# Kernel tuning notes

Hardware: AMD Instinct MI355X
Metric: run time of the kernel (lower is better)

Reference implementation:

```python
import jax, jax.numpy as jnp
import numpy as np

B, TQ, TK, D, H = 8, 1024, 1024, 1024, 16
HD = D // H
EPS = 1e-5


def layernorm(x, g, b):
    mu = jnp.mean(x, axis=-1, keepdims=True)
    var = jnp.mean(jnp.square(x - mu), axis=-1, keepdims=True)
    return (x - mu) * jax.lax.rsqrt(var + EPS) * g + b


def setup_inputs() -> dict:
    key = jax.random.key(0)
    ks = jax.random.split(key, 16)
    s = 1.0 / np.sqrt(D)
    return {
        "base": jax.random.normal(ks[0], (B, TQ, D), jnp.float32),
        "fusion": jax.random.normal(ks[1], (B, TK, D), jnp.float32),
        "Wq": jax.random.normal(ks[2], (D, D), jnp.float32) * s,
        "Wk": jax.random.normal(ks[3], (D, D), jnp.float32) * s,
        "Wv": jax.random.normal(ks[4], (D, D), jnp.float32) * s,
        "Wo": jax.random.normal(ks[5], (D, D), jnp.float32) * s,
        "g1": jnp.ones((D,), jnp.float32),
        "b1": jnp.zeros((D,), jnp.float32),
        "g2": jnp.ones((D,), jnp.float32),
        "b2": jnp.zeros((D,), jnp.float32),
        "fc1_w": jax.random.normal(ks[6], (D, D), jnp.float32) * s,
        "fc1_b": jnp.zeros((D,), jnp.float32),
        "fc2_w": jax.random.normal(ks[7], (D, D), jnp.float32) * s,
        "fc2_b": jnp.zeros((D,), jnp.float32),
        "rw": jax.random.normal(ks[8], (D, D), jnp.float32) * s,
        "rb": jnp.zeros((D,), jnp.float32),
        "alpha": jnp.asarray(0.1, jnp.float32),
    }


def reference(base, fusion, Wq, Wk, Wv, Wo, g1, b1, g2, b2,
              fc1_w, fc1_b, fc2_w, fc2_b, rw, rb, alpha):
    def split_heads(x):  # [B,T,D] -> [B,H,T,hd]
        return x.reshape(B, -1, H, HD).transpose(0, 2, 1, 3)

    Q = split_heads(base @ Wq.T)
    K = split_heads(fusion @ Wk.T)
    V = split_heads(fusion @ Wv.T)

    scores = jnp.einsum("bhqd,bhkd->bhqk", Q, K) / jnp.sqrt(jnp.float32(HD))
    attn = jax.nn.softmax(scores, axis=-1)
    # threshold mask (the torch scatter_ with arange indices is an identity copy)
    masked = attn * (attn >= alpha).astype(attn.dtype)
    # second softmax over masked weights (zeros contribute exp(0)=1, as in the original)
    attn2 = jax.nn.softmax(masked, axis=-1)
    out = jnp.einsum("bhqk,bhkd->bhqd", attn2, V)
    out = out.transpose(0, 2, 1, 3).reshape(B, TQ, D)
    out = out @ Wo.T
    x = layernorm(base + out, g1, b1)  # dropout is eval-mode identity
    ff = jax.nn.silu(jax.nn.silu(x @ fc1_w.T + fc1_b) @ fc2_w.T + fc2_b)
    y = layernorm(x + ff, g2, b2)
    final = y @ rw.T + rb
    return final, masked
```

## Files before the change

### kernel.cpp

```cpp
#include <hip/hip_runtime.h>


typedef unsigned short u16;
typedef __attribute__((ext_vector_type(8))) short  bf16x8;
typedef __attribute__((ext_vector_type(4))) short  s16x4;
typedef __attribute__((ext_vector_type(4))) float  f32x4;

#define GLL16(gp, lp) __builtin_amdgcn_global_load_lds(                     \
    (__attribute__((address_space(1))) const void*)(gp),                    \
    (__attribute__((address_space(3))) void*)(lp), 16, 0, 0)

__device__ __forceinline__ u16 f2bf(float x) {
  union { float f; unsigned u; } v; v.f = x;
  return (u16)((v.u + 0x7FFF + ((v.u >> 16) & 1)) >> 16);
}
__device__ __forceinline__ float bf2f(u16 h) {
  union { unsigned u; float f; } v; v.u = ((unsigned)h) << 16;
  return v.f;
}
__device__ __forceinline__ f32x4 zero4() { f32x4 z = {0.f, 0.f, 0.f, 0.f}; return z; }

__global__ __launch_bounds__(256) void pack_act(const float* __restrict__ a,
                                                const float* __restrict__ b,
                                                u16* __restrict__ outa,
                                                u16* __restrict__ outb) {
  size_t i = (size_t)blockIdx.x * 256 + threadIdx.x;
  const f32x4* in = (const f32x4*)(blockIdx.y ? b : a);
  s16x4* out = (s16x4*)(blockIdx.y ? outb : outa);
  f32x4 v = in[i];
  s16x4 o;
  o[0] = (short)f2bf(v[0]); o[1] = (short)f2bf(v[1]);
  o[2] = (short)f2bf(v[2]); o[3] = (short)f2bf(v[3]);
  out[i] = o;
}

__global__ __launch_bounds__(256) void pack_w(
    const float* __restrict__ w0, const float* __restrict__ w1,
    const float* __restrict__ w2, const float* __restrict__ w3,
    const float* __restrict__ w4, const float* __restrict__ w5,
    const float* __restrict__ w6, u16* __restrict__ out) {
  size_t i = (size_t)blockIdx.x * 256 + threadIdx.x;
  const float* in;
  switch (blockIdx.y) {
    case 0: in = w0; break;  case 1: in = w1; break;
    case 2: in = w2; break;  case 3: in = w3; break;
    case 4: in = w4; break;  case 5: in = w5; break;
    default: in = w6; break;
  }
  f32x4 v = ((const f32x4*)in)[i];
  s16x4 o;
  o[0] = (short)f2bf(v[0]); o[1] = (short)f2bf(v[1]);
  o[2] = (short)f2bf(v[2]); o[3] = (short)f2bf(v[3]);
  ((s16x4*)(out + (size_t)blockIdx.y * 1048576))[i] = o;
}

#define EPI_QKV       0
#define EPI_BF16      1
#define EPI_SILU_BF16 4
#define EPI_BIAS_F32  6

template <int EPI>
__global__ __launch_bounds__(256) void gemm_bt(
    const u16* __restrict__ A, int lda,
    const u16* __restrict__ W, int ldw,
    int M, int N, int K,
    float* __restrict__ outF, u16* __restrict__ outU,
    const float* __restrict__ bias,
    const u16* __restrict__ A2) {
  __shared__ u16 As[2][128 * 32];
  __shared__ u16 Bs[2][128 * 32];
  int tid = threadIdx.x;
  int l = tid & 63, w = tid >> 6;
  int wr = w >> 1, wc = w & 1, lr = l & 15, lq = l >> 4;

  int fid = blockIdx.y * 8 + blockIdx.x;
  int swz = (fid & 7) * 64 + (fid >> 3);
  int m0 = (swz >> 3) * 128, n0 = (swz & 7) * 128;

  const u16* Ap = A;
  const u16* Wp = W;
  u16* outUp = outU;
  if constexpr (EPI == EPI_QKV) {
    int z = blockIdx.z;
    if (z) Ap = A2;
    Wp = W + (size_t)z * 1048576;
    outUp = outU + (size_t)z * 8388608;
  }

  f32x4 acc[4][4];
#pragma unroll
  for (int i = 0; i < 4; i++)
#pragma unroll
    for (int j = 0; j < 4; j++) acc[i][j] = zero4();

  auto stage = [&](const u16* src, int ld, int r0, int k0, u16* lds) {
#pragma unroll
    for (int j = 0; j < 2; ++j) {
      int seg = j * 256 + tid;
      int row = seg >> 2, sp = seg & 3;
      const u16* g = src + (size_t)(r0 + row) * ld + k0 +
                     ((sp ^ ((row >> 1) & 3)) << 3);
      GLL16(g, lds + seg * 8);
    }
  };

  int nk = K >> 5;
  stage(Ap, lda, m0, 0, As[0]);
  stage(Wp, ldw, n0, 0, Bs[0]);
  for (int kt = 0; kt < nk; ++kt) {
    __syncthreads();
    if (kt + 1 < nk) {
      stage(Ap, lda, m0, (kt + 1) << 5, As[(kt + 1) & 1]);
      stage(Wp, ldw, n0, (kt + 1) << 5, Bs[(kt + 1) & 1]);
    }
    const u16* Ab = As[kt & 1];
    const u16* Bb = Bs[kt & 1];
    bf16x8 af[4], bw[4];
    int slot = (lq ^ ((lr >> 1) & 3)) << 3;
#pragma unroll
    for (int mi = 0; mi < 4; mi++)
      af[mi] = *(const bf16x8*)&Ab[(wr * 64 + mi * 16 + lr) * 32 + slot];
#pragma unroll
    for (int ni = 0; ni < 4; ni++)
      bw[ni] = *(const bf16x8*)&Bb[(wc * 64 + ni * 16 + lr) * 32 + slot];
#pragma unroll
    for (int mi = 0; mi < 4; mi++)
#pragma unroll
      for (int ni = 0; ni < 4; ni++)
        acc[mi][ni] = __builtin_amdgcn_mfma_f32_16x16x32_bf16(af[mi], bw[ni],
                                                              acc[mi][ni], 0, 0, 0);
  }

#pragma unroll
  for (int mi = 0; mi < 4; mi++) {
#pragma unroll
    for (int ni = 0; ni < 4; ni++) {
      int col = n0 + wc * 64 + ni * 16 + lr;
#pragma unroll
      for (int r = 0; r < 4; r++) {
        int row = m0 + wr * 64 + mi * 16 + lq * 4 + r;
        float v = acc[mi][ni][r];
        if constexpr (EPI == EPI_QKV) {
          int b = row >> 10, t = row & 1023, h = col >> 6, d = col & 63;
          int z = blockIdx.z;
          if (z == 0) {
            outUp[((size_t)(b * 16 + h) * 1024 + t) * 64 + d] = f2bf(v);
          } else if (z == 1) {
            size_t base = ((size_t)(b * 16 + h) * 1024 + t) * 64;
            outUp[base + (((d >> 3) ^ (t & 7)) << 3) + (d & 7)] = f2bf(v);
          } else {
            size_t o = ((size_t)(b * 16 + h) * 64 + d) * 1024 + (t & ~63) +
                       ((((t >> 3) & 7) ^ (d & 7)) << 3) + (t & 7);
            outUp[o] = f2bf(v);
          }
        } else if constexpr (EPI == EPI_BF16) {
          outUp[(size_t)row * N + col] = f2bf(v);
        } else if constexpr (EPI == EPI_SILU_BF16) {
          float z = v + bias[col];
          outUp[(size_t)row * N + col] = f2bf(z / (1.f + __expf(-z)));
        } else {
          outF[(size_t)row * N + col] = v + bias[col];
        }
      }
    }
  }
}

template <int EPI>
__global__ __launch_bounds__(512) void gemm_bt8(
    const u16* __restrict__ A, int lda,
    const u16* __restrict__ W, int ldw,
    int M, int N, int K,
    float* __restrict__ outF, u16* __restrict__ outU,
    const float* __restrict__ bias) {
  __shared__ u16 As[2][128 * 32];
  __shared__ u16 Bs[2][128 * 32];
  int tid = threadIdx.x;
  int l = tid & 63, w = tid >> 6;
  int wr = w >> 2, wc = w & 3, lr = l & 15, lq = l >> 4;

  int fid = blockIdx.y * 8 + blockIdx.x;
  int swz = (fid & 7) * 64 + (fid >> 3);
  int m0 = (swz >> 3) * 128, n0 = (swz & 7) * 128;

  f32x4 acc[4][2];
#pragma unroll
  for (int i = 0; i < 4; i++)
#pragma unroll
    for (int j = 0; j < 2; j++) acc[i][j] = zero4();

  auto stage = [&](const u16* src, int ld, int r0, int k0, u16* lds) {
    int seg = tid;
    int row = seg >> 2, sp = seg & 3;
    const u16* g = src + (size_t)(r0 + row) * ld + k0 +
                   ((sp ^ ((row >> 1) & 3)) << 3);
    GLL16(g, lds + seg * 8);
  };

  int nk = K >> 5;
  stage(A, lda, m0, 0, As[0]);
  stage(W, ldw, n0, 0, Bs[0]);
  for (int kt = 0; kt < nk; ++kt) {
    __syncthreads();
    if (kt + 1 < nk) {
      stage(A, lda, m0, (kt + 1) << 5, As[(kt + 1) & 1]);
      stage(W, ldw, n0, (kt + 1) << 5, Bs[(kt + 1) & 1]);
    }
    const u16* Ab = As[kt & 1];
    const u16* Bb = Bs[kt & 1];
    bf16x8 af[4], bw[2];
    int slot = (lq ^ ((lr >> 1) & 3)) << 3;
#pragma unroll
    for (int mi = 0; mi < 4; mi++)
      af[mi] = *(const bf16x8*)&Ab[(wr * 64 + mi * 16 + lr) * 32 + slot];
#pragma unroll
    for (int ni = 0; ni < 2; ni++)
      bw[ni] = *(const bf16x8*)&Bb[(wc * 32 + ni * 16 + lr) * 32 + slot];
#pragma unroll
    for (int mi = 0; mi < 4; mi++)
#pragma unroll
      for (int ni = 0; ni < 2; ni++)
        acc[mi][ni] = __builtin_amdgcn_mfma_f32_16x16x32_bf16(af[mi], bw[ni],
                                                              acc[mi][ni], 0, 0, 0);
  }

#pragma unroll
  for (int mi = 0; mi < 4; mi++) {
#pragma unroll
    for (int ni = 0; ni < 2; ni++) {
      int col = n0 + wc * 32 + ni * 16 + lr;
#pragma unroll
      for (int r = 0; r < 4; r++) {
        int row = m0 + wr * 64 + mi * 16 + lq * 4 + r;
        float v = acc[mi][ni][r];
        if constexpr (EPI == EPI_BF16) {
          outU[(size_t)row * N + col] = f2bf(v);
        } else if constexpr (EPI == EPI_SILU_BF16) {
          float z = v + bias[col];
          outU[(size_t)row * N + col] = f2bf(z / (1.f + __expf(-z)));
        } else {
          outF[(size_t)row * N + col] = v + bias[col];
        }
      }
    }
  }
}

__global__ __launch_bounds__(256) void attn_kernel(
    const u16* __restrict__ Q2, const u16* __restrict__ K2,
    const u16* __restrict__ Vt, const float* __restrict__ alphap,
    float* __restrict__ masked_out, u16* __restrict__ attn_out) {
  __shared__ __align__(16) u16 Ks[2][4096];
  __shared__ __align__(16) u16 Vs[2][4096];
  __shared__ __align__(16) u16 Ps[4][2][16 * 72];

  int tid = threadIdx.x;
  int l = tid & 63, w = tid >> 6, lr = l & 15, lq = l >> 4;

  int bid = blockIdx.x;
  int qi  = bid >> 7;
  int bh  = (bid & 7) * 16 + ((bid >> 3) & 15);
  int h = bh & 15, b = bh >> 4;
  int q0 = qi * 128;

  const u16* Qb = Q2 + (size_t)bh * 1024 * 64;
  const u16* Kb = K2 + (size_t)bh * 1024 * 64;
  const u16* Vb = Vt + (size_t)bh * 64 * 1024;
  float alpha = alphap[0];
  int qw = q0 + w * 32;

  auto stageK = [&](int kc, u16* dst) {
#pragma unroll
    for (int j = 0; j < 2; ++j) {
      int seg = j * 256 + tid;
      GLL16(Kb + (size_t)kc * 4096 + seg * 8, dst + seg * 8);
    }
  };
  auto stageV = [&](int kc, u16* dst) {
#pragma unroll
    for (int j = 0; j < 2; ++j) {
      int seg = j * 256 + tid;
      GLL16(Vb + (size_t)(seg >> 3) * 1024 + kc * 64 + (seg & 7) * 8, dst + seg * 8);
    }
  };

  bf16x8 qf[2][2];
#pragma unroll
  for (int s = 0; s < 2; s++)
#pragma unroll
    for (int kt = 0; kt < 2; kt++)
      qf[s][kt] = *(const bf16x8*)(Qb + (size_t)(qw + s * 16 + lr) * 64 + kt * 32 + lq * 8);

  float s1[2][4] = {{0.f, 0.f, 0.f, 0.f}, {0.f, 0.f, 0.f, 0.f}};

  stageK(0, Ks[0]);
  for (int kc = 0; kc < 16; ++kc) {
    __syncthreads();
    if (kc + 1 < 16) stageK(kc + 1, Ks[(kc + 1) & 1]);
    const u16* Kc = Ks[kc & 1];
    f32x4 acc[2][4];
#pragma unroll
    for (int s = 0; s < 2; s++)
#pragma unroll
      for (int ni = 0; ni < 4; ni++) acc[s][ni] = zero4();
    __builtin_amdgcn_s_setprio(1);
#pragma unroll
    for (int ni = 0; ni < 4; ++ni) {
      int t = ni * 16 + lr;
      bf16x8 k0 = *(const bf16x8*)&Kc[t * 64 + (((0 + lq) ^ (lr & 7)) << 3)];
      bf16x8 k1 = *(const bf16x8*)&Kc[t * 64 + (((4 + lq) ^ (lr & 7)) << 3)];
#pragma unroll
      for (int s = 0; s < 2; s++) {
        acc[s][ni] = __builtin_amdgcn_mfma_f32_16x16x32_bf16(qf[s][0], k0, acc[s][ni], 0, 0, 0);
        acc[s][ni] = __builtin_amdgcn_mfma_f32_16x16x32_bf16(qf[s][1], k1, acc[s][ni], 0, 0, 0);
      }
    }
    __builtin_amdgcn_s_setprio(0);
#pragma unroll
    for (int s = 0; s < 2; s++)
#pragma unroll
      for (int ni = 0; ni < 4; ni++)
#pragma unroll
        for (int r = 0; r < 4; r++)
          s1[s][r] += __expf(acc[s][ni][r] * 0.125f);
  }
#pragma unroll
  for (int s = 0; s < 2; s++)
#pragma unroll
    for (int r = 0; r < 4; r++) {
      float v = s1[s][r];
      v += __shfl_xor(v, 1); v += __shfl_xor(v, 2);
      v += __shfl_xor(v, 4); v += __shfl_xor(v, 8);
      s1[s][r] = 1.0f / v;
    }

  float s2[2][4] = {{0.f, 0.f, 0.f, 0.f}, {0.f, 0.f, 0.f, 0.f}};
  f32x4 oacc[2][4];
#pragma unroll
  for (int s = 0; s < 2; s++)
#pragma unroll
    for (int dg = 0; dg < 4; dg++) oacc[s][dg] = zero4();

  stageK(0, Ks[0]);
  stageV(0, Vs[0]);
  for (int kc = 0; kc < 16; ++kc) {
    if (kc == 0) {
      asm volatile("s_waitcnt vmcnt(0) lgkmcnt(0)" ::: "memory");
    } else {
      asm volatile("s_waitcnt vmcnt(32) lgkmcnt(0)" ::: "memory");
    }
    __builtin_amdgcn_s_barrier();
    __builtin_amdgcn_sched_barrier(0);
    if (kc + 1 < 16) {
      stageK(kc + 1, Ks[(kc + 1) & 1]);
      stageV(kc + 1, Vs[(kc + 1) & 1]);
    }
    const u16* Kc = Ks[kc & 1];
    const u16* Vc = Vs[kc & 1];

    f32x4 acc[2][4];
#pragma unroll
    for (int s = 0; s < 2; s++)
#pragma unroll
      for (int ni = 0; ni < 4; ni++) acc[s][ni] = zero4();
    __builtin_amdgcn_s_setprio(1);
#pragma unroll
    for (int ni = 0; ni < 4; ++ni) {
      int t = ni * 16 + lr;
      bf16x8 k0 = *(const bf16x8*)&Kc[t * 64 + (((0 + lq) ^ (lr & 7)) << 3)];
      bf16x8 k1 = *(const bf16x8*)&Kc[t * 64 + (((4 + lq) ^ (lr & 7)) << 3)];
#pragma unroll
      for (int s = 0; s < 2; s++) {
        acc[s][ni] = __builtin_amdgcn_mfma_f32_16x16x32_bf16(qf[s][0], k0, acc[s][ni], 0, 0, 0);
        acc[s][ni] = __builtin_amdgcn_mfma_f32_16x16x32_bf16(qf[s][1], k1, acc[s][ni], 0, 0, 0);
      }
    }
    __builtin_amdgcn_s_setprio(0);

#pragma unroll
    for (int s = 0; s < 2; s++) {
#pragma unroll
      for (int ni = 0; ni < 4; ni++) {
#pragma unroll
        for (int r = 0; r < 4; r++) {
          float e = __expf(acc[s][ni][r] * 0.125f);
          float a = e * s1[s][r];
          a = (a >= alpha) ? a : 0.0f;
          size_t row = (size_t)bh * 1024 + qw + s * 16 + lq * 4 + r;
          masked_out[row * 1024 + kc * 64 + ni * 16 + lr] = a;
          float p = __expf(a);
          s2[s][r] += p;
          Ps[w][s][(lq * 4 + r) * 72 + ni * 16 + lr] = f2bf(p);
        }
      }
    }
    asm volatile("s_waitcnt lgkmcnt(0)" ::: "memory");

    bf16x8 pf[2][2];
#pragma unroll
    for (int s = 0; s < 2; s++)
#pragma unroll
      for (int kt = 0; kt < 2; kt++)
        pf[s][kt] = *(const bf16x8*)&Ps[w][s][lr * 72 + kt * 32 + lq * 8];
    __builtin_amdgcn_s_setprio(1);
#pragma unroll
    for (int dg = 0; dg < 4; dg++) {
      int d = dg * 16 + lr;
      bf16x8 v0 = *(const bf16x8*)&Vc[d * 64 + (((0 + lq) ^ (lr & 7)) << 3)];
      bf16x8 v1 = *(const bf16x8*)&Vc[d * 64 + (((4 + lq) ^ (lr & 7)) << 3)];
#pragma unroll
      for (int s = 0; s < 2; s++) {
        oacc[s][dg] = __builtin_amdgcn_mfma_f32_16x16x32_bf16(pf[s][0], v0, oacc[s][dg], 0, 0, 0);
        oacc[s][dg] = __builtin_amdgcn_mfma_f32_16x16x32_bf16(pf[s][1], v1, oacc[s][dg], 0, 0, 0);
      }
    }
    __builtin_amdgcn_s_setprio(0);
  }

#pragma unroll
  for (int s = 0; s < 2; s++)
#pragma unroll
    for (int r = 0; r < 4; r++) {
      float v = s2[s][r];
      v += __shfl_xor(v, 1); v += __shfl_xor(v, 2);
      v += __shfl_xor(v, 4); v += __shfl_xor(v, 8);
      s2[s][r] = 1.0f / v;
    }
#pragma unroll
  for (int s = 0; s < 2; s++)
#pragma unroll
    for (int dg = 0; dg < 4; dg++)
#pragma unroll
      for (int r = 0; r < 4; r++) {
        int q = qw + s * 16 + lq * 4 + r;
        attn_out[(size_t)(b * 1024 + q) * 1024 + h * 64 + dg * 16 + lr] =
            f2bf(oacc[s][dg][r] * s2[s][r]);
      }
}

__global__ __launch_bounds__(256) void ln_kernel(
    const float* __restrict__ A, const u16* __restrict__ Bv,
    const float* __restrict__ g, const float* __restrict__ beta,
    float* __restrict__ outF, u16* __restrict__ outB) {
  __shared__ float red[4];
  int row = blockIdx.x, t = threadIdx.x;
  const float* pa = A + (size_t)row * 1024;
  const u16* pb = Bv + (size_t)row * 1024;
  float v[4];
  float s = 0.f;
#pragma unroll
  for (int i = 0; i < 4; i++) {
    int c = t + 256 * i;
    v[i] = pa[c] + bf2f(pb[c]);
    s += v[i];
  }
#pragma unroll
  for (int off = 1; off < 64; off <<= 1) s += __shfl_xor(s, off);
  if ((t & 63) == 0) red[t >> 6] = s;
  __syncthreads();
  s = red[0] + red[1] + red[2] + red[3];
  float mu = s * 0.0009765625f;
  float q = 0.f;
#pragma unroll
  for (int i = 0; i < 4; i++) { float d = v[i] - mu; q += d * d; }
  __syncthreads();
#pragma unroll
  for (int off = 1; off < 64; off <<= 1) q += __shfl_xor(q, off);
  if ((t & 63) == 0) red[t >> 6] = q;
  __syncthreads();
  q = red[0] + red[1] + red[2] + red[3];
  float rs = rsqrtf(q * 0.0009765625f + 1e-5f);
#pragma unroll
  for (int i = 0; i < 4; i++) {
    int c = t + 256 * i;
    float y = (v[i] - mu) * rs * g[c] + beta[c];
    if (outF) outF[(size_t)row * 1024 + c] = y;
    if (outB) outB[(size_t)row * 1024 + c] = f2bf(y);
  }
}

#define WS_BASEB   0
#define WS_FUSB    16777216
#define WS_W       33554432
#define WS_QKV     48234496
#define WS_ATTNO   98566144
#define WS_X       115343360
#define WS_OB      WS_FUSB
#define WS_XB      WS_BASEB
#define WS_H1      WS_ATTNO
#define WS_FFB     WS_QKV
#define WS_YB      (WS_QKV + 16777216)

extern "C" void kernel_launch(void* const* d_in, const int* in_sizes, int n_in,
                              void* d_out, int out_size, void* d_ws, size_t ws_size,
                              hipStream_t stream) {
  const float* base   = (const float*)d_in[0];
  const float* fusion = (const float*)d_in[1];
  const float* Wq     = (const float*)d_in[2];
  const float* Wk     = (const float*)d_in[3];
  const float* Wv     = (const float*)d_in[4];
  const float* Wo     = (const float*)d_in[5];
  const float* g1     = (const float*)d_in[6];
  const float* b1     = (const float*)d_in[7];
  const float* g2     = (const float*)d_in[8];
  const float* b2     = (const float*)d_in[9];
  const float* fc1w   = (const float*)d_in[10];
  const float* fc1b   = (const float*)d_in[11];
  const float* fc2w   = (const float*)d_in[12];
  const float* fc2b   = (const float*)d_in[13];
  const float* rw     = (const float*)d_in[14];
  const float* rb     = (const float*)d_in[15];
  const float* alphap = (const float*)d_in[16];

  char* ws = (char*)d_ws;
  u16* baseb  = (u16*)(ws + WS_BASEB);
  u16* fusb   = (u16*)(ws + WS_FUSB);
  u16* wall   = (u16*)(ws + WS_W);
  u16* Q2     = (u16*)(ws + WS_QKV);
  u16* attno  = (u16*)(ws + WS_ATTNO);
  u16* obufb  = (u16*)(ws + WS_OB);
  float* x    = (float*)(ws + WS_X);
  u16* xb     = (u16*)(ws + WS_XB);
  u16* h1     = (u16*)(ws + WS_H1);
  u16* ffb    = (u16*)(ws + WS_FFB);
  u16* yb     = (u16*)(ws + WS_YB);

  float* final_out  = (float*)d_out;
  float* masked_out = final_out + 8388608;

  pack_act<<<dim3(8192, 2), 256, 0, stream>>>(base, fusion, baseb, fusb);
  pack_w<<<dim3(1024, 7), 256, 0, stream>>>(Wq, Wk, Wv, Wo, fc1w, fc2w, rw, wall);

  dim3 gg(8, 64);

  gemm_bt<EPI_QKV><<<dim3(8, 64, 3), 256, 0, stream>>>(
      baseb, 1024, wall, 1024, 8192, 1024, 1024, nullptr, Q2, nullptr, fusb);

  attn_kernel<<<dim3(1024), 256, 0, stream>>>(
      Q2, Q2 + 8388608, Q2 + 16777216, alphap, masked_out, attno);

  gemm_bt8<EPI_BF16><<<gg, 512, 0, stream>>>(attno, 1024, wall + 3 * 1048576, 1024,
                                             8192, 1024, 1024, nullptr, obufb, nullptr);
  ln_kernel<<<8192, 256, 0, stream>>>(base, obufb, g1, b1, x, xb);

  gemm_bt8<EPI_SILU_BF16><<<gg, 512, 0, stream>>>(xb, 1024, wall + 4 * 1048576, 1024,
                                                  8192, 1024, 1024, nullptr, h1, fc1b);
  gemm_bt8<EPI_SILU_BF16><<<gg, 512, 0, stream>>>(h1, 1024, wall + 5 * 1048576, 1024,
                                                  8192, 1024, 1024, nullptr, ffb, fc2b);
  ln_kernel<<<8192, 256, 0, stream>>>(x, ffb, g2, b2, nullptr, yb);

  gemm_bt8<EPI_BIAS_F32><<<gg, 512, 0, stream>>>(yb, 1024, wall + 6 * 1048576, 1024,
                                                 8192, 1024, 1024, final_out, nullptr, rb);
}
```

Measured before the change: 977.2 us.

## Double GEMM K-tile and split attention across eight waves per block

The bt8 GEMM now stages 64-wide K tiles with an 8-way XOR swizzle, halving the number of barrier/pipeline iterations per output tile. The attention kernel uses 512 threads with each wave owning 16 query rows instead of 32, adjusting staging, wait counts and the P scratch buffer. This aims to raise occupancy and latency hiding in attention and reduce sync overhead in the GEMMs, at the cost of more LDS per GEMM block and lower per-wave reuse of K/V fragments in attention.

```diff
diff --git a/kernel.cpp b/kernel.cpp
--- a/kernel.cpp
+++ b/kernel.cpp
@@ -173,8 +173,8 @@
     int M, int N, int K,
     float* __restrict__ outF, u16* __restrict__ outU,
     const float* __restrict__ bias) {
-  __shared__ u16 As[2][128 * 32];
-  __shared__ u16 Bs[2][128 * 32];
+  __shared__ u16 As[2][128 * 64];
+  __shared__ u16 Bs[2][128 * 64];
   int tid = threadIdx.x;
   int l = tid & 63, w = tid >> 6;
   int wr = w >> 2, wc = w & 3, lr = l & 15, lq = l >> 4;
@@ -190,38 +190,46 @@
     for (int j = 0; j < 2; j++) acc[i][j] = zero4();
 
   auto stage = [&](const u16* src, int ld, int r0, int k0, u16* lds) {
-    int seg = tid;
-    int row = seg >> 2, sp = seg & 3;
-    const u16* g = src + (size_t)(r0 + row) * ld + k0 +
-                   ((sp ^ ((row >> 1) & 3)) << 3);
-    GLL16(g, lds + seg * 8);
+#pragma unroll
+    for (int j = 0; j < 2; ++j) {
+      int seg = j * 512 + tid;
+      int row = seg >> 3, sp = seg & 7;
+      const u16* g = src + (size_t)(r0 + row) * ld + k0 +
+                     ((sp ^ (row & 7)) << 3);
+      GLL16(g, lds + seg * 8);
+    }
   };
 
-  int nk = K >> 5;
+  int nk = K >> 6;
   stage(A, lda, m0, 0, As[0]);
   stage(W, ldw, n0, 0, Bs[0]);
   for (int kt = 0; kt < nk; ++kt) {
     __syncthreads();
     if (kt + 1 < nk) {
-      stage(A, lda, m0, (kt + 1) << 5, As[(kt + 1) & 1]);
-      stage(W, ldw, n0, (kt + 1) << 5, Bs[(kt + 1) & 1]);
+      stage(A, lda, m0, (kt + 1) << 6, As[(kt + 1) & 1]);
+      stage(W, ldw, n0, (kt + 1) << 6, Bs[(kt + 1) & 1]);
     }
     const u16* Ab = As[kt & 1];
     const u16* Bb = Bs[kt & 1];
-    bf16x8 af[4], bw[2];
-    int slot = (lq ^ ((lr >> 1) & 3)) << 3;
-#pragma unroll
-    for (int mi = 0; mi < 4; mi++)
-      af[mi] = *(const bf16x8*)&Ab[(wr * 64 + mi * 16 + lr) * 32 + slot];
-#pragma unroll
-    for (int ni = 0; ni < 2; ni++)
-      bw[ni] = *(const bf16x8*)&Bb[(wc * 32 + ni * 16 + lr) * 32 + slot];
-#pragma unroll
-    for (int mi = 0; mi < 4; mi++)
+    bf16x8 af[4][2], bw[2][2];
+#pragma unroll
+    for (int kk = 0; kk < 2; kk++) {
+      int slot = ((kk * 4 + lq) ^ (lr & 7)) << 3;
+#pragma unroll
+      for (int mi = 0; mi < 4; mi++)
+        af[mi][kk] = *(const bf16x8*)&Ab[(wr * 64 + mi * 16 + lr) * 64 + slot];
 #pragma unroll
       for (int ni = 0; ni < 2; ni++)
-        acc[mi][ni] = __builtin_amdgcn_mfma_f32_16x16x32_bf16(af[mi], bw[ni],
-                                                              acc[mi][ni], 0, 0, 0);
+        bw[ni][kk] = *(const bf16x8*)&Bb[(wc * 32 + ni * 16 + lr) * 64 + slot];
+    }
+#pragma unroll
+    for (int kk = 0; kk < 2; kk++)
+#pragma unroll
+      for (int mi = 0; mi < 4; mi++)
+#pragma unroll
+        for (int ni = 0; ni < 2; ni++)
+          acc[mi][ni] = __builtin_amdgcn_mfma_f32_16x16x32_bf16(
+              af[mi][kk], bw[ni][kk], acc[mi][ni], 0, 0, 0);
   }
 
 #pragma unroll
@@ -246,13 +254,13 @@
   }
 }
 
-__global__ __launch_bounds__(256) void attn_kernel(
+__global__ __launch_bounds__(512) void attn_kernel(
     const u16* __restrict__ Q2, const u16* __restrict__ K2,
     const u16* __restrict__ Vt, const float* __restrict__ alphap,
     float* __restrict__ masked_out, u16* __restrict__ attn_out) {
   __shared__ __align__(16) u16 Ks[2][4096];
   __shared__ __align__(16) u16 Vs[2][4096];
-  __shared__ __align__(16) u16 Ps[4][2][16 * 72];
+  __shared__ __align__(16) u16 Ps[8][16 * 72];
 
   int tid = threadIdx.x;
   int l = tid & 63, w = tid >> 6, lr = l & 15, lq = l >> 4;
@@ -267,79 +275,60 @@
   const u16* Kb = K2 + (size_t)bh * 1024 * 64;
   const u16* Vb = Vt + (size_t)bh * 64 * 1024;
   float alpha = alphap[0];
-  int qw = q0 + w * 32;
+  int qw = q0 + w * 16;
 
   auto stageK = [&](int kc, u16* dst) {
-#pragma unroll
-    for (int j = 0; j < 2; ++j) {
-      int seg = j * 256 + tid;
-      GLL16(Kb + (size_t)kc * 4096 + seg * 8, dst + seg * 8);
-    }
+    int seg = tid;
+    GLL16(Kb + (size_t)kc * 4096 + seg * 8, dst + seg * 8);
   };
   auto stageV = [&](int kc, u16* dst) {
-#pragma unroll
-    for (int j = 0; j < 2; ++j) {
-      int seg = j * 256 + tid;
-      GLL16(Vb + (size_t)(seg >> 3) * 1024 + kc * 64 + (seg & 7) * 8, dst + seg * 8);
-    }
+    int seg = tid;
+    GLL16(Vb + (size_t)(seg >> 3) * 1024 + kc * 64 + (seg & 7) * 8, dst + seg * 8);
   };
 
-  bf16x8 qf[2][2];
-#pragma unroll
-  for (int s = 0; s < 2; s++)
-#pragma unroll
-    for (int kt = 0; kt < 2; kt++)
-      qf[s][kt] = *(const bf16x8*)(Qb + (size_t)(qw + s * 16 + lr) * 64 + kt * 32 + lq * 8);
-
-  float s1[2][4] = {{0.f, 0.f, 0.f, 0.f}, {0.f, 0.f, 0.f, 0.f}};
+  bf16x8 qf[2];
+#pragma unroll
+  for (int kt = 0; kt < 2; kt++)
+    qf[kt] = *(const bf16x8*)(Qb + (size_t)(qw + lr) * 64 + kt * 32 + lq * 8);
+
+  float s1[4] = {0.f, 0.f, 0.f, 0.f};
 
   stageK(0, Ks[0]);
   for (int kc = 0; kc < 16; ++kc) {
     __syncthreads();
     if (kc + 1 < 16) stageK(kc + 1, Ks[(kc + 1) & 1]);
     const u16* Kc = Ks[kc & 1];
-    f32x4 acc[2][4];
-#pragma unroll
-    for (int s = 0; s < 2; s++)
-#pragma unroll
-      for (int ni = 0; ni < 4; ni++) acc[s][ni] = zero4();
+    f32x4 acc[4];
+#pragma unroll
+    for (int ni = 0; ni < 4; ni++) acc[ni] = zero4();
     __builtin_amdgcn_s_setprio(1);
 #pragma unroll
     for (int ni = 0; ni < 4; ++ni) {
       int t = ni * 16 + lr;
       bf16x8 k0 = *(const bf16x8*)&Kc[t * 64 + (((0 + lq) ^ (lr & 7)) << 3)];
       bf16x8 k1 = *(const bf16x8*)&Kc[t * 64 + (((4 + lq) ^ (lr & 7)) << 3)];
-#pragma unroll
-      for (int s = 0; s < 2; s++) {
-        acc[s][ni] = __builtin_amdgcn_mfma_f32_16x16x32_bf16(qf[s][0], k0, acc[s][ni], 0, 0, 0);
-        acc[s][ni] = __builtin_amdgcn_mfma_f32_16x16x32_bf16(qf[s][1], k1, acc[s][ni], 0, 0, 0);
-      }
+      acc[ni] = __builtin_amdgcn_mfma_f32_16x16x32_bf16(qf[0], k0, acc[ni], 0, 0, 0);
+      acc[ni] = __builtin_amdgcn_mfma_f32_16x16x32_bf16(qf[1], k1, acc[ni], 0, 0, 0);
     }
     __builtin_amdgcn_s_setprio(0);
 #pragma unroll
-    for (int s = 0; s < 2; s++)
-#pragma unroll
-      for (int ni = 0; ni < 4; ni++)
-#pragma unroll
-        for (int r = 0; r < 4; r++)
-          s1[s][r] += __expf(acc[s][ni][r] * 0.125f);
-  }
-#pragma unroll
-  for (int s = 0; s < 2; s++)
-#pragma unroll
-    for (int r = 0; r < 4; r++) {
-      float v = s1[s][r];
-      v += __shfl_xor(v, 1); v += __shfl_xor(v, 2);
-      v += __shfl_xor(v, 4); v += __shfl_xor(v, 8);
-      s1[s][r] = 1.0f / v;
-    }
-
-  float s2[2][4] = {{0.f, 0.f, 0.f, 0.f}, {0.f, 0.f, 0.f, 0.f}};
-  f32x4 oacc[2][4];
-#pragma unroll
-  for (int s = 0; s < 2; s++)
-#pragma unroll
-    for (int dg = 0; dg < 4; dg++) oacc[s][dg] = zero4();
+    for (int ni = 0; ni < 4; ni++)
+#pragma unroll
+      for (int r = 0; r < 4; r++)
+        s1[r] += __expf(acc[ni][r] * 0.125f);
+  }
+#pragma unroll
+  for (int r = 0; r < 4; r++) {
+    float v = s1[r];
+    v += __shfl_xor(v, 1); v += __shfl_xor(v, 2);
+    v += __shfl_xor(v, 4); v += __shfl_xor(v, 8);
+    s1[r] = 1.0f / v;
+  }
+
+  float s2[4] = {0.f, 0.f, 0.f, 0.f};
+  f32x4 oacc[4];
+#pragma unroll
+  for (int dg = 0; dg < 4; dg++) oacc[dg] = zero4();
 
   stageK(0, Ks[0]);
   stageV(0, Vs[0]);
@@ -347,7 +336,7 @@
     if (kc == 0) {
       asm volatile("s_waitcnt vmcnt(0) lgkmcnt(0)" ::: "memory");
     } else {
-      asm volatile("s_waitcnt vmcnt(32) lgkmcnt(0)" ::: "memory");
+      asm volatile("s_waitcnt vmcnt(16) lgkmcnt(0)" ::: "memory");
     }
     __builtin_amdgcn_s_barrier();
     __builtin_amdgcn_sched_barrier(0);
@@ -358,84 +347,67 @@
     const u16* Kc = Ks[kc & 1];
     const u16* Vc = Vs[kc & 1];
 
-    f32x4 acc[2][4];
-#pragma unroll
-    for (int s = 0; s < 2; s++)
-#pragma unroll
-      for (int ni = 0; ni < 4; ni++) acc[s][ni] = zero4();
+    f32x4 acc[4];
+#pragma unroll
+    for (int ni = 0; ni < 4; ni++) acc[ni] = zero4();
     __builtin_amdgcn_s_setprio(1);
 #pragma unroll
     for (int ni = 0; ni < 4; ++ni) {
       int t = ni * 16 + lr;
       bf16x8 k0 = *(const bf16x8*)&Kc[t * 64 + (((0 + lq) ^ (lr & 7)) << 3)];
       bf16x8 k1 = *(const bf16x8*)&Kc[t * 64 + (((4 + lq) ^ (lr & 7)) << 3)];
-#pragma unroll
-      for (int s = 0; s < 2; s++) {
-        acc[s][ni] = __builtin_amdgcn_mfma_f32_16x16x32_bf16(qf[s][0], k0, acc[s][ni], 0, 0, 0);
-        acc[s][ni] = __builtin_amdgcn_mfma_f32_16x16x32_bf16(qf[s][1], k1, acc[s][ni], 0, 0, 0);
+      acc[ni] = __builtin_amdgcn_mfma_f32_16x16x32_bf16(qf[0], k0, acc[ni], 0, 0, 0);
+      acc[ni] = __builtin_amdgcn_mfma_f32_16x16x32_bf16(qf[1], k1, acc[ni], 0, 0, 0);
+    }
+    __builtin_amdgcn_s_setprio(0);
+
+#pragma unroll
+    for (int ni = 0; ni < 4; ni++) {
+#pragma unroll
+      for (int r = 0; r < 4; r++) {
+        float e = __expf(acc[ni][r] * 0.125f);
+        float a = e * s1[r];
+        a = (a >= alpha) ? a : 0.0f;
+        size_t row = (size_t)bh * 1024 + qw + lq * 4 + r;
+        masked_out[row * 1024 + kc * 64 + ni * 16 + lr] = a;
+        float p = __expf(a);
+        s2[r] += p;
+        Ps[w][(lq * 4 + r) * 72 + ni * 16 + lr] = f2bf(p);
       }
     }
-    __builtin_amdgcn_s_setprio(0);
-
-#pragma unroll
-    for (int s = 0; s < 2; s++) {
-#pragma unroll
-      for (int ni = 0; ni < 4; ni++) {
-#pragma unroll
-        for (int r = 0; r < 4; r++) {
-          float e = __expf(acc[s][ni][r] * 0.125f);
-          float a = e * s1[s][r];
-          a = (a >= alpha) ? a : 0.0f;
-          size_t row = (size_t)bh * 1024 + qw + s * 16 + lq * 4 + r;
-          masked_out[row * 1024 + kc * 64 + ni * 16 + lr] = a;
-          float p = __expf(a);
-          s2[s][r] += p;
-          Ps[w][s][(lq * 4 + r) * 72 + ni * 16 + lr] = f2bf(p);
-        }
-      }
-    }
     asm volatile("s_waitcnt lgkmcnt(0)" ::: "memory");
 
-    bf16x8 pf[2][2];
-#pragma unroll
-    for (int s = 0; s < 2; s++)
-#pragma unroll
-      for (int kt = 0; kt < 2; kt++)
-        pf[s][kt] = *(const bf16x8*)&Ps[w][s][lr * 72 + kt * 32 + lq * 8];
+    bf16x8 pf[2];
+#pragma unroll
+    for (int kt = 0; kt < 2; kt++)
+      pf[kt] = *(const bf16x8*)&Ps[w][lr * 72 + kt * 32 + lq * 8];
     __builtin_amdgcn_s_setprio(1);
 #pragma unroll
     for (int dg = 0; dg < 4; dg++) {
       int d = dg * 16 + lr;
       bf16x8 v0 = *(const bf16x8*)&Vc[d * 64 + (((0 + lq) ^ (lr & 7)) << 3)];
       bf16x8 v1 = *(const bf16x8*)&Vc[d * 64 + (((4 + lq) ^ (lr & 7)) << 3)];
-#pragma unroll
-      for (int s = 0; s < 2; s++) {
-        oacc[s][dg] = __builtin_amdgcn_mfma_f32_16x16x32_bf16(pf[s][0], v0, oacc[s][dg], 0, 0, 0);
-        oacc[s][dg] = __builtin_amdgcn_mfma_f32_16x16x32_bf16(pf[s][1], v1, oacc[s][dg], 0, 0, 0);
-      }
+      oacc[dg] = __builtin_amdgcn_mfma_f32_16x16x32_bf16(pf[0], v0, oacc[dg], 0, 0, 0);
+      oacc[dg] = __builtin_amdgcn_mfma_f32_16x16x32_bf16(pf[1], v1, oacc[dg], 0, 0, 0);
     }
     __builtin_amdgcn_s_setprio(0);
   }
 
 #pragma unroll
-  for (int s = 0; s < 2; s++)
+  for (int r = 0; r < 4; r++) {
+    float v = s2[r];
+    v += __shfl_xor(v, 1); v += __shfl_xor(v, 2);
+    v += __shfl_xor(v, 4); v += __shfl_xor(v, 8);
+    s2[r] = 1.0f / v;
+  }
+#pragma unroll
+  for (int dg = 0; dg < 4; dg++)
 #pragma unroll
     for (int r = 0; r < 4; r++) {
-      float v = s2[s][r];
-      v += __shfl_xor(v, 1); v += __shfl_xor(v, 2);
-      v += __shfl_xor(v, 4); v += __shfl_xor(v, 8);
-      s2[s][r] = 1.0f / v;
-    }
-#pragma unroll
-  for (int s = 0; s < 2; s++)
-#pragma unroll
-    for (int dg = 0; dg < 4; dg++)
-#pragma unroll
-      for (int r = 0; r < 4; r++) {
-        int q = qw + s * 16 + lq * 4 + r;
-        attn_out[(size_t)(b * 1024 + q) * 1024 + h * 64 + dg * 16 + lr] =
-            f2bf(oacc[s][dg][r] * s2[s][r]);
-      }
+      int q = qw + lq * 4 + r;
+      attn_out[(size_t)(b * 1024 + q) * 1024 + h * 64 + dg * 16 + lr] =
+          f2bf(oacc[dg][r] * s2[r]);
+    }
 }
 
 __global__ __launch_bounds__(256) void ln_kernel(
@@ -536,7 +508,7 @@
   gemm_bt<EPI_QKV><<<dim3(8, 64, 3), 256, 0, stream>>>(
       baseb, 1024, wall, 1024, 8192, 1024, 1024, nullptr, Q2, nullptr, fusb);
 
-  attn_kernel<<<dim3(1024), 256, 0, stream>>>(
+  attn_kernel<<<dim3(1024), 512, 0, stream>>>(
       Q2, Q2 + 8388608, Q2 + 16777216, alphap, masked_out, attno);
 
   gemm_bt8<EPI_BF16><<<gg, 512, 0, stream>>>(attno, 1024, wall + 3 * 1048576, 1024,
```

After: 939.8 us. 1.04x faster.
